# Optimization experiments

Hardware: AMD Instinct MI355X
Metric: run time of the kernel (lower is better)

Reference implementation:

```python
import jax, jax.numpy as jnp
import numpy as np
import math

B, T, D = 4, 4096, 512
K_CACHE = 16

def _layernorm(x, g, b, eps=1e-5):
    mu = x.mean(-1, keepdims=True)
    var = ((x - mu) ** 2).mean(-1, keepdims=True)
    return (x - mu) / jnp.sqrt(var + eps) * g + b

def _shift1(x):
    # prepend zero along time axis, drop last: x_prev[t] = x[t-1]
    return jnp.pad(x, ((0, 0), (1, 0), (0, 0)))[:, :-1]

def mipt_parallel_scan(p, theta, inp_re, inp_im):
    # Faithful replication of the torch loop: ceil(log2(T+1)) iterations,
    # each combining with the element shifted by ONE position (as written).
    Bt, Tt, Dt = p.shape
    a_re = (1.0 - p) * jnp.cos(theta)
    a_im = (1.0 - p) * jnp.sin(theta)
    b_re, b_im = inp_re, inp_im
    mask = (jnp.arange(Tt) >= 1)[None, :, None]
    steps = math.ceil(math.log2(Tt + 1))
    for _ in range(steps):
        ar_p, ai_p = _shift1(a_re), _shift1(a_im)
        br_p, bi_p = _shift1(b_re), _shift1(b_im)
        new_a_re = a_re * ar_p - a_im * ai_p
        new_a_im = a_re * ai_p + a_im * ar_p
        new_b_re = a_re * br_p - a_im * bi_p + b_re
        new_b_im = a_re * bi_p + a_im * br_p + b_im
        a_re = jnp.where(mask, new_a_re, a_re)
        a_im = jnp.where(mask, new_a_im, a_im)
        b_re = jnp.where(mask, new_b_re, b_re)
        b_im = jnp.where(mask, new_b_im, b_im)
    return b_re, b_im

def setup_inputs() -> dict:
    key = jax.random.key(0)
    ks = jax.random.split(key, 32)
    s = 0.02
    def W(k, i, o):
        return jax.random.normal(k, (i, o), jnp.float32) * s
    inp = {
        'x': jax.random.normal(ks[0], (B, T, D), jnp.float32),
        'ln1_g': jnp.ones((D,), jnp.float32), 'ln1_b': jnp.zeros((D,), jnp.float32),
        'ln2_g': jnp.ones((D,), jnp.float32), 'ln2_b': jnp.zeros((D,), jnp.float32),
        'Wp_w': W(ks[1], D, D), 'Wp_b': jnp.zeros((D,), jnp.float32),
        'Wt_w': W(ks[2], D, D), 'Wt_b': jnp.zeros((D,), jnp.float32),
        'Wr_w': W(ks[3], D, D), 'Wr_b': jnp.zeros((D,), jnp.float32),
        'Wi_w': W(ks[4], D, D), 'Wi_b': jnp.zeros((D,), jnp.float32),
        'Wk_w': W(ks[5], D, D), 'Wk_b': jnp.zeros((D,), jnp.float32),
        'Wv_w': W(ks[6], D, D), 'Wv_b': jnp.zeros((D,), jnp.float32),
        'Wq_w': W(ks[7], D, D), 'Wq_b': jnp.zeros((D,), jnp.float32),
        'gate_w': W(ks[8], D, 1), 'gate_b': jnp.zeros((1,), jnp.float32),
        'ffn1_w': W(ks[9], D, 4 * D), 'ffn1_b': jnp.zeros((4 * D,), jnp.float32),
        'ffn2_w': W(ks[10], 4 * D, D), 'ffn2_b': jnp.zeros((D,), jnp.float32),
    }
    return inp

def reference(x, ln1_g, ln1_b, ln2_g, ln2_b, Wp_w, Wp_b, Wt_w, Wt_b, Wr_w, Wr_b,
              Wi_w, Wi_b, Wk_w, Wk_b, Wv_w, Wv_b, Wq_w, Wq_b, gate_w, gate_b,
              ffn1_w, ffn1_b, ffn2_w, ffn2_b):
    Bx, Tx, Dx = x.shape
    residual = x
    xn = _layernorm(x, ln1_g, ln1_b)
    p = jax.nn.sigmoid(xn @ Wp_w + Wp_b)
    theta = xn @ Wt_w + Wt_b
    inp_re = xn @ Wr_w + Wr_b
    inp_im = xn @ Wi_w + Wi_b
    h_re, _h_im = mipt_parallel_scan(p, theta, inp_re, inp_im)
    h_mean = h_re.mean(axis=1)  # [B, D]
    # CausalSparseCache (eval mode)
    p_scalar = p.mean(axis=-1)  # [B, T]
    K = min(K_CACHE, Tx)
    _, topk_idx = jax.lax.top_k(p_scalar, K)  # [B, K]
    idx = jnp.broadcast_to(topk_idx[:, :, None], (Bx, K, Dx))
    h_topk = jnp.take_along_axis(h_re, idx, axis=1)  # [B, K, D]
    keys = h_topk @ Wk_w + Wk_b
    values = h_topk @ Wv_w + Wv_b
    query = (h_mean @ Wq_w + Wq_b)[:, None, :]  # [B, 1, D]
    scores = jnp.einsum('bqd,bkd->bqk', query, keys) / math.sqrt(Dx)
    attn = jax.nn.softmax(scores, axis=-1)
    cache_out = jnp.einsum('bqk,bkd->bqd', attn, values)[:, 0]  # [B, D]
    g = jax.nn.sigmoid(h_mean @ gate_w + gate_b)  # [B, 1]
    out = h_mean + g * cache_out
    h = h_re + residual
    hn = _layernorm(h, ln2_g, ln2_b)
    ffn = jax.nn.gelu(hn @ ffn1_w + ffn1_b, approximate=False) @ ffn2_w + ffn2_b
    h = h + ffn
    return (h, out)
```

## Files before the change

### kernel.cpp

```cpp
#include <hip/hip_runtime.h>
#include <hip/hip_bf16.h>
#include <cstdint>
#include <cstddef>

typedef __bf16 bf16;
typedef __attribute__((ext_vector_type(8))) __bf16 bf16x8;
typedef __attribute__((ext_vector_type(4))) float f32x4;

#define BB 4
#define TT 4096
#define DD 512
#define MM (BB * TT)
#define OUT1_OFF ((size_t)MM * DD)

typedef __attribute__((address_space(1))) void as1_void;
typedef __attribute__((address_space(3))) void as3_void;

__device__ __forceinline__ void gl_lds16(const void* g, void* l) {
    __builtin_amdgcn_global_load_lds((as1_void*)(uintptr_t)g,
                                     (as3_void*)(uintptr_t)l, 16, 0, 0);
}

__global__ void transpose_bf16(const float* __restrict__ in, bf16* __restrict__ out,
                               int R, int C) {
    __shared__ float tile[32][33];
    const int c0 = blockIdx.x * 32, r0 = blockIdx.y * 32;
    const int tx = threadIdx.x, ty = threadIdx.y;
#pragma unroll
    for (int i = 0; i < 32; i += 8)
        tile[ty + i][tx] = in[(size_t)(r0 + ty + i) * C + (c0 + tx)];
    __syncthreads();
#pragma unroll
    for (int i = 0; i < 32; i += 8)
        out[(size_t)(c0 + ty + i) * R + (r0 + tx)] = (bf16)tile[tx][ty + i];
}

__global__ void pack_bias(const float* __restrict__ a, const float* __restrict__ b,
                          const float* __restrict__ c, const float* __restrict__ d,
                          float* __restrict__ o) {
    const int i = blockIdx.x * 256 + threadIdx.x;
    if (i < 2048) {
        const float* s = (i < 512) ? a : (i < 1024) ? b : (i < 1536) ? c : d;
        o[i] = s[i & 511];
    }
}

__global__ void zero_kernel(float* __restrict__ p, int n) {
    const int i = blockIdx.x * 256 + threadIdx.x;
    if (i < n) p[i] = 0.f;
}

__global__ __launch_bounds__(256) void ln_kernel(
    const float* __restrict__ X, const float* __restrict__ Xadd,
    const float* __restrict__ gw, const float* __restrict__ bw,
    bf16* __restrict__ out) {
    const int row = blockIdx.x * 4 + (threadIdx.x >> 6);
    const int lane = threadIdx.x & 63;
    const float* xr = X + (size_t)row * DD + lane * 8;
    float v[8];
    float4 v0 = *(const float4*)xr;
    float4 v1 = *(const float4*)(xr + 4);
    v[0] = v0.x; v[1] = v0.y; v[2] = v0.z; v[3] = v0.w;
    v[4] = v1.x; v[5] = v1.y; v[6] = v1.z; v[7] = v1.w;
    if (Xadd) {
        const float* ad = Xadd + (size_t)row * DD + lane * 8;
        float4 a0 = *(const float4*)ad;
        float4 a1 = *(const float4*)(ad + 4);
        v[0] += a0.x; v[1] += a0.y; v[2] += a0.z; v[3] += a0.w;
        v[4] += a1.x; v[5] += a1.y; v[6] += a1.z; v[7] += a1.w;
    }
    float s = 0.f, ss = 0.f;
#pragma unroll
    for (int i = 0; i < 8; ++i) { s += v[i]; ss += v[i] * v[i]; }
#pragma unroll
    for (int o = 32; o; o >>= 1) { s += __shfl_down(s, o); ss += __shfl_down(ss, o); }
    s = __shfl(s, 0); ss = __shfl(ss, 0);
    const float mu = s * (1.f / DD);
    const float var = ss * (1.f / DD) - mu * mu;
    const float rstd = rsqrtf(var + 1e-5f);
    bf16x8 o8;
#pragma unroll
    for (int i = 0; i < 8; ++i)
        o8[i] = (bf16)((v[i] - mu) * rstd * gw[lane * 8 + i] + bw[lane * 8 + i]);
    *(bf16x8*)(out + (size_t)row * DD + lane * 8) = o8;
}

template <int MODE>
__global__ __launch_bounds__(256) void gemm_bt(
    const bf16* __restrict__ A, const bf16* __restrict__ Bt,
    const float* __restrict__ bias, void* __restrict__ Cout,
    void* __restrict__ Cout2,
    const float* __restrict__ add1, const float* __restrict__ add2,
    int M, int N, int K) {
    __shared__ bf16 As[2][4096];
    __shared__ bf16 Bs[2][4096];
    const int tid = threadIdx.x;
    const int lane = tid & 63;
    const int wv = tid >> 6;
    const int wr = wv >> 1, wc = wv & 1;
    const int nb = N >> 7;
    const int nwg = gridDim.x;
    int bx = blockIdx.x;
    if ((nwg & 7) == 0) bx = (bx & 7) * (nwg >> 3) + (bx >> 3);
    const int bm = bx / nb, bn = bx % nb;
    const int m0 = bm << 7, n0 = bn << 7;

    const int srow = tid >> 2;
    const int scol = (tid & 3) << 3;
    const bf16* Asrc = A + (size_t)(m0 + srow) * K + scol;
    const bf16* Bsrc = Bt + (size_t)(n0 + srow) * K + scol;
    const size_t rstep = (size_t)64 * K;

    const int lr = lane & 15, lg = lane >> 4;
    const int aoff = (wr * 64 + lr) * 32 + lg * 8;
    const int boff = (wc * 64 + lr) * 32 + lg * 8;

#define STG(buf, k0)                                                \
    do {                                                            \
        gl_lds16(Asrc + (k0),         &As[buf][wv * 512]);          \
        gl_lds16(Asrc + (k0) + rstep, &As[buf][wv * 512 + 2048]);   \
        gl_lds16(Bsrc + (k0),         &Bs[buf][wv * 512]);          \
        gl_lds16(Bsrc + (k0) + rstep, &Bs[buf][wv * 512 + 2048]);   \
    } while (0)

    f32x4 acc00 = {}, acc01 = {}, acc02 = {}, acc03 = {};
    f32x4 acc10 = {}, acc11 = {}, acc12 = {}, acc13 = {};
    f32x4 acc20 = {}, acc21 = {}, acc22 = {}, acc23 = {};
    f32x4 acc30 = {}, acc31 = {}, acc32 = {}, acc33 = {};

    const int NT = K >> 5;
    STG(0, 0);
    STG(1, 32);
    for (int t = 0; t < NT; ++t) {
        if (t + 1 < NT) asm volatile("s_waitcnt vmcnt(4)" ::: "memory");
        else            asm volatile("s_waitcnt vmcnt(0)" ::: "memory");
        __builtin_amdgcn_s_barrier();
        asm volatile("" ::: "memory");
        const bf16* Ab = As[t & 1];
        const bf16* Bb = Bs[t & 1];
        bf16x8 af0 = *(const bf16x8*)&Ab[aoff];
        bf16x8 af1 = *(const bf16x8*)&Ab[aoff + 512];
        bf16x8 af2 = *(const bf16x8*)&Ab[aoff + 1024];
        bf16x8 af3 = *(const bf16x8*)&Ab[aoff + 1536];
        bf16x8 bf0 = *(const bf16x8*)&Bb[boff];
        bf16x8 bf1 = *(const bf16x8*)&Bb[boff + 512];
        bf16x8 bf2 = *(const bf16x8*)&Bb[boff + 1024];
        bf16x8 bf3 = *(const bf16x8*)&Bb[boff + 1536];
#define MF(a_, b_, c_) c_ = __builtin_amdgcn_mfma_f32_16x16x32_bf16(a_, b_, c_, 0, 0, 0)
        MF(af0, bf0, acc00); MF(af0, bf1, acc01); MF(af0, bf2, acc02); MF(af0, bf3, acc03);
        MF(af1, bf0, acc10); MF(af1, bf1, acc11); MF(af1, bf2, acc12); MF(af1, bf3, acc13);
        MF(af2, bf0, acc20); MF(af2, bf1, acc21); MF(af2, bf2, acc22); MF(af2, bf3, acc23);
        MF(af3, bf0, acc30); MF(af3, bf1, acc31); MF(af3, bf2, acc32); MF(af3, bf3, acc33);
#undef MF
        __builtin_amdgcn_s_barrier();
        asm volatile("" ::: "memory");
        if (t + 2 < NT) STG(t & 1, (t + 2) << 5);
    }
#undef STG

#define EPI(mi, ni, ACC)                                                        \
    do {                                                                        \
        const int gmb = m0 + wr * 64 + mi * 16 + 4 * lg;                        \
        const int gn = n0 + wc * 64 + ni * 16 + lr;                             \
        const float bia = bias[gn];                                             \
        _Pragma("unroll")                                                       \
        for (int i = 0; i < 4; ++i) {                                           \
            float v = ACC[i] + bia;                                             \
            const int row = gmb + i;                                            \
            if (MODE == 0) {                                                    \
                if (gn < 512) ((float*)Cout)[(size_t)row * 512 + gn] = v;       \
                else ((bf16*)Cout2)[(size_t)row * 1536 + (gn - 512)] = (bf16)v; \
            } else if (MODE == 1) {                                             \
                const float ge = 0.5f * v * (1.0f + erff(v * 0.70710678118654752f)); \
                ((bf16*)Cout)[(size_t)row * N + gn] = (bf16)ge;                 \
            } else {                                                            \
                const size_t off = (size_t)row * N + gn;                        \
                ((float*)Cout)[off] = v + add1[off] + add2[off];                \
            }                                                                   \
        }                                                                       \
    } while (0)
    EPI(0, 0, acc00); EPI(0, 1, acc01); EPI(0, 2, acc02); EPI(0, 3, acc03);
    EPI(1, 0, acc10); EPI(1, 1, acc11); EPI(1, 2, acc12); EPI(1, 3, acc13);
    EPI(2, 0, acc20); EPI(2, 1, acc21); EPI(2, 2, acc22); EPI(2, 3, acc23);
    EPI(3, 0, acc30); EPI(3, 1, acc31); EPI(3, 2, acc32); EPI(3, 3, acc33);
#undef EPI
}

__global__ __launch_bounds__(256) void pscalar_kernel(const float* __restrict__ linp,
                                                      float* __restrict__ ps) {
    const int row = blockIdx.x * 4 + (threadIdx.x >> 6);
    const int lane = threadIdx.x & 63;
    const float* pr = linp + (size_t)row * 512 + lane * 8;
    float s = 0.f;
#pragma unroll
    for (int i = 0; i < 8; ++i) {
        const float v = pr[i];
        s += __builtin_amdgcn_rcpf(1.f + __expf(-v));
    }
#pragma unroll
    for (int o = 32; o; o >>= 1) s += __shfl_down(s, o);
    if (!lane) ps[row] = s * (1.f / 512.f);
}

#define SCL 32
__global__ __launch_bounds__(256) void scan_kernel(const float* __restrict__ linp,
                                                   const bf16* __restrict__ lint,
                                                   float* __restrict__ h_re) {
    const int blk = blockIdx.x;
    const int dh = blk & 1;
    const int tc = (blk >> 1) & 127;
    const int b = blk >> 8;
    const int d = dh * 256 + threadIdx.x;
    const int t0 = tc * SCL;

    float par[13], pai[13], pbr[13], pbi[13];
#pragma unroll
    for (int k = 0; k < 13; ++k) { par[k] = 0.f; pai[k] = 0.f; pbr[k] = 0.f; pbi[k] = 0.f; }

    const int warm = (tc == 0) ? 0 : 13;
    const float* pp = linp + (size_t)(b * TT + t0 - warm) * 512 + d;
    const bf16* tp = lint + (size_t)(b * TT + t0 - warm) * 1536 + d;
    float* pout = h_re + ((size_t)(b * TT + t0)) * DD + d;

    for (int s = 0; s < warm; ++s) {
        const float pl = pp[0];
        const float th = (float)tp[0];
        const float re = (float)tp[512];
        const float im = (float)tp[1024];
        pp += 512; tp += 1536;
        const float om = __builtin_amdgcn_rcpf(1.f + __expf(pl));
        const float sn = __sinf(th), cs = __cosf(th);
        float car = om * cs, cai = om * sn, cbr = re, cbi = im;
#pragma unroll
        for (int k = 0; k < 13; ++k) {
            const float tar = par[k], tai = pai[k], tbr = pbr[k], tbi = pbi[k];
            par[k] = car; pai[k] = cai; pbr[k] = cbr; pbi[k] = cbi;
            const float nbr = car * tbr - cai * tbi + cbr;
            const float nbi = car * tbi + cai * tbr + cbi;
            if (k < 12) {
                const float nar = car * tar - cai * tai;
                const float nai = car * tai + cai * tar;
                car = nar; cai = nai;
            }
            cbr = nbr; cbi = nbi;
        }
    }

#pragma unroll 4
    for (int s = 0; s < SCL; ++s) {
        const int t = t0 + s;
        const float pl = pp[0];
        const float th = (float)tp[0];
        const float re = (float)tp[512];
        const float im = (float)tp[1024];
        pp += 512; tp += 1536;
        const float om = __builtin_amdgcn_rcpf(1.f + __expf(pl));
        const float sn = __sinf(th), cs = __cosf(th);
        float car = om * cs, cai = om * sn, cbr = re, cbi = im;
        if (t == 0) {
#pragma unroll
            for (int k = 0; k < 13; ++k) { par[k] = car; pai[k] = cai; pbr[k] = cbr; pbi[k] = cbi; }
        } else {
#pragma unroll
            for (int k = 0; k < 13; ++k) {
                const float tar = par[k], tai = pai[k], tbr = pbr[k], tbi = pbi[k];
                par[k] = car; pai[k] = cai; pbr[k] = cbr; pbi[k] = cbi;
                const float nbr = car * tbr - cai * tbi + cbr;
                const float nbi = car * tbi + cai * tbr + cbi;
                if (k < 12) {
                    const float nar = car * tar - cai * tai;
                    const float nai = car * tai + cai * tar;
                    car = nar; cai = nai;
                }
                cbr = nbr; cbi = nbi;
            }
        }
        pout[(size_t)s * DD] = cbr;
    }
}

__global__ __launch_bounds__(256) void hmean_kernel(const float* __restrict__ h_re,
                                                    float* __restrict__ hsum) {
    const int blk = blockIdx.x;
    const int b = blk >> 6;
    const int dh = (blk >> 5) & 1;
    const int tc = blk & 31;
    const int d = dh * 256 + threadIdx.x;
    float s = 0.f;
    const float* p = h_re + ((size_t)(b * TT + tc * 128)) * DD + d;
    for (int t = 0; t < 128; ++t) s += p[(size_t)t * DD];
    atomicAdd(&hsum[b * DD + d], s);
}

__global__ __launch_bounds__(256) void topk_kernel(const float* __restrict__ ps,
                                                   int* __restrict__ idx_out) {
    __shared__ float vals[TT];
    __shared__ float rv[4];
    __shared__ int ri[4];
    const int b = blockIdx.x, tid = threadIdx.x;
    for (int i = tid; i < TT; i += 256) vals[i] = ps[b * TT + i];
    __syncthreads();
    for (int kk = 0; kk < 16; ++kk) {
        float bv = -1e30f; int bi = 0x7fffffff;
        for (int i = tid; i < TT; i += 256) {
            const float v = vals[i];
            if (v > bv || (v == bv && i < bi)) { bv = v; bi = i; }
        }
#pragma unroll
        for (int o = 32; o; o >>= 1) {
            const float ov = __shfl_down(bv, o);
            const int oi = __shfl_down(bi, o);
            if (ov > bv || (ov == bv && oi < bi)) { bv = ov; bi = oi; }
        }
        const int lane = tid & 63, wid = tid >> 6;
        if (!lane) { rv[wid] = bv; ri[wid] = bi; }
        __syncthreads();
        if (!tid) {
            float fbv = rv[0]; int fbi = ri[0];
            for (int w = 1; w < 4; ++w)
                if (rv[w] > fbv || (rv[w] == fbv && ri[w] < fbi)) { fbv = rv[w]; fbi = ri[w]; }
            idx_out[b * 16 + kk] = fbi;
            vals[fbi] = -1e30f;
        }
        __syncthreads();
    }
}

__global__ __launch_bounds__(256) void kv_kernel(
    const float* __restrict__ h_re, const int* __restrict__ tki,
    const float* __restrict__ Wk, const float* __restrict__ Wkb,
    const float* __restrict__ Wv, const float* __restrict__ Wvb,
    float* __restrict__ keys, float* __restrict__ vals) {
    const int blk = blockIdx.x;
    const int b = blk >> 4, j = blk & 15;
    const int tid = threadIdx.x;
    __shared__ float hrow[512];
    const int row = tki[b * 16 + j];
    for (int i = tid; i < 512; i += 256)
        hrow[i] = h_re[((size_t)(b * TT + row)) * DD + i];
    __syncthreads();
    for (int n = tid; n < 512; n += 256) {
        float sk = Wkb[n], sv = Wvb[n];
        for (int k = 0; k < 512; ++k) {
            const float h = hrow[k];
            sk += h * Wk[(size_t)k * 512 + n];
            sv += h * Wv[(size_t)k * 512 + n];
        }
        keys[((size_t)(b * 16 + j)) * 512 + n] = sk;
        vals[((size_t)(b * 16 + j)) * 512 + n] = sv;
    }
}

__global__ __launch_bounds__(256) void attn_out_kernel(
    const float* __restrict__ hsum, const float* __restrict__ Wq,
    const float* __restrict__ Wqb, const float* __restrict__ gw,
    const float* __restrict__ gb, const float* __restrict__ keys,
    const float* __restrict__ vals, float* __restrict__ out1) {
    const int b = blockIdx.x, tid = threadIdx.x;
    const int lane = tid & 63, wid = tid >> 6;
    __shared__ float hm[512];
    __shared__ float q[512];
    __shared__ float sc[16];
    __shared__ float red[4];
    for (int d0 = tid; d0 < 512; d0 += 256)
        hm[d0] = hsum[b * 512 + d0] * (1.f / 4096.f);
    __syncthreads();
    for (int n = tid; n < 512; n += 256) {
        float s = Wqb[n];
        for (int k = 0; k < 512; ++k) s += hm[k] * Wq[(size_t)k * 512 + n];
        q[n] = s;
    }
    float gp = 0.f;
    for (int k = tid; k < 512; k += 256) gp += hm[k] * gw[k];
#pragma unroll
    for (int o = 32; o; o >>= 1) gp += __shfl_down(gp, o);
    if (!lane) red[wid] = gp;
    __syncthreads();
    const float g = 1.f / (1.f + __expf(-(red[0] + red[1] + red[2] + red[3] + gb[0])));
    for (int kk = wid; kk < 16; kk += 4) {
        float sp = 0.f;
        const float* kr = keys + ((size_t)(b * 16 + kk)) * 512;
        for (int k2 = lane; k2 < 512; k2 += 64) sp += q[k2] * kr[k2];
#pragma unroll
        for (int o = 32; o; o >>= 1) sp += __shfl_down(sp, o);
        if (!lane) sc[kk] = sp * 0.04419417382415922f;
    }
    __syncthreads();
    float mx = sc[0];
#pragma unroll
    for (int kk = 1; kk < 16; ++kk) mx = fmaxf(mx, sc[kk]);
    float den = 0.f;
    float w16[16];
#pragma unroll
    for (int kk = 0; kk < 16; ++kk) { w16[kk] = __expf(sc[kk] - mx); den += w16[kk]; }
    const float rden = 1.f / den;
    for (int d0 = tid; d0 < 512; d0 += 256) {
        float co = 0.f;
#pragma unroll
        for (int kk = 0; kk < 16; ++kk)
            co += w16[kk] * vals[((size_t)(b * 16 + kk)) * 512 + d0];
        out1[b * 512 + d0] = hm[d0] + g * (co * rden);
    }
}

extern "C" void kernel_launch(void* const* d_in, const int* in_sizes, int n_in,
                              void* d_out, int out_size, void* d_ws, size_t ws_size,
                              hipStream_t stream) {
    const float* x    = (const float*)d_in[0];
    const float* ln1g = (const float*)d_in[1];
    const float* ln1b = (const float*)d_in[2];
    const float* ln2g = (const float*)d_in[3];
    const float* ln2b = (const float*)d_in[4];
    const float* Wp_w = (const float*)d_in[5];
    const float* Wp_b = (const float*)d_in[6];
    const float* Wt_w = (const float*)d_in[7];
    const float* Wt_b = (const float*)d_in[8];
    const float* Wr_w = (const float*)d_in[9];
    const float* Wr_b = (const float*)d_in[10];
    const float* Wi_w = (const float*)d_in[11];
    const float* Wi_b = (const float*)d_in[12];
    const float* Wk_w = (const float*)d_in[13];
    const float* Wk_b = (const float*)d_in[14];
    const float* Wv_w = (const float*)d_in[15];
    const float* Wv_b = (const float*)d_in[16];
    const float* Wq_w = (const float*)d_in[17];
    const float* Wq_b = (const float*)d_in[18];
    const float* gw   = (const float*)d_in[19];
    const float* gb   = (const float*)d_in[20];
    const float* f1w  = (const float*)d_in[21];
    const float* f1b  = (const float*)d_in[22];
    const float* f2w  = (const float*)d_in[23];
    const float* f2b  = (const float*)d_in[24];

    char* wsp = (char*)d_ws;
    float* linp = (float*)wsp;
    bf16* lint = (bf16*)(wsp + 33554432);
    char* p = wsp + 83886080;
    float* h_re = (float*)p; p += 33554432;
    bf16* xn = (bf16*)p;     p += 16777216;
    bf16* hn = (bf16*)p;     p += 16777216;
    bf16* wcat = (bf16*)p;   p += 2097152;
    bf16* f1bt = (bf16*)p;   p += 2097152;
    bf16* f2bt = (bf16*)p;   p += 2097152;
    float* bcat = (float*)p; p += 8192;
    float* ps = (float*)p;   p += 65536;
    float* hsum = (float*)p; p += 8192;
    int* tki = (int*)p;      p += 256;
    float* keys = (float*)p; p += 131072;
    float* valsb = (float*)p;
    bf16* act = (bf16*)wsp;
    float* out0 = (float*)d_out;
    float* out1 = (float*)d_out + OUT1_OFF;

    dim3 tb(32, 8);
    transpose_bf16<<<dim3(16, 16), tb, 0, stream>>>(Wp_w, wcat + (size_t)0 * 512 * 512, 512, 512);
    transpose_bf16<<<dim3(16, 16), tb, 0, stream>>>(Wt_w, wcat + (size_t)1 * 512 * 512, 512, 512);
    transpose_bf16<<<dim3(16, 16), tb, 0, stream>>>(Wr_w, wcat + (size_t)2 * 512 * 512, 512, 512);
    transpose_bf16<<<dim3(16, 16), tb, 0, stream>>>(Wi_w, wcat + (size_t)3 * 512 * 512, 512, 512);
    transpose_bf16<<<dim3(64, 16), tb, 0, stream>>>(f1w, f1bt, 512, 2048);
    transpose_bf16<<<dim3(16, 64), tb, 0, stream>>>(f2w, f2bt, 2048, 512);
    pack_bias<<<8, 256, 0, stream>>>(Wp_b, Wt_b, Wr_b, Wi_b, bcat);

    ln_kernel<<<4096, 256, 0, stream>>>(x, nullptr, ln1g, ln1b, xn);
    gemm_bt<0><<<2048, 256, 0, stream>>>(xn, wcat, bcat, linp, lint, nullptr, nullptr, MM, 2048, 512);
    pscalar_kernel<<<4096, 256, 0, stream>>>(linp, ps);
    scan_kernel<<<1024, 256, 0, stream>>>(linp, lint, h_re);
    zero_kernel<<<8, 256, 0, stream>>>(hsum, 2048);
    hmean_kernel<<<256, 256, 0, stream>>>(h_re, hsum);
    topk_kernel<<<4, 256, 0, stream>>>(ps, tki);
    kv_kernel<<<64, 256, 0, stream>>>(h_re, tki, Wk_w, Wk_b, Wv_w, Wv_b, keys, valsb);
    attn_out_kernel<<<4, 256, 0, stream>>>(hsum, Wq_w, Wq_b, gw, gb, keys, valsb, out1);
    ln_kernel<<<4096, 256, 0, stream>>>(h_re, x, ln2g, ln2b, hn);
    gemm_bt<1><<<2048, 256, 0, stream>>>(hn, f1bt, f1b, act, nullptr, nullptr, nullptr, MM, 2048, 512);
    gemm_bt<2><<<512, 256, 0, stream>>>(act, f2bt, f2b, out0, nullptr, h_re, x, MM, 512, 2048);
}
```

Baseline: 432.9 us.

## Add 256x256 8-wave GEMM kernel, halve scan chunk length, use hardware sin/cos

After: 494.6 us. 14.2% more time.

```diff
diff --git a/kernel.cpp b/kernel.cpp
--- a/kernel.cpp
+++ b/kernel.cpp
@@ -83,6 +83,124 @@
     for (int i = 0; i < 8; ++i)
         o8[i] = (bf16)((v[i] - mu) * rstd * gw[lane * 8 + i] + bw[lane * 8 + i]);
     *(bf16x8*)(out + (size_t)row * DD + lane * 8) = o8;
+}
+
+#define MF(a_, b_, c_) c_ = __builtin_amdgcn_mfma_f32_16x16x32_bf16(a_, b_, c_, 0, 0, 0)
+
+template <int MODE>
+__global__ __launch_bounds__(512, 2) void gemm8p(
+    const bf16* __restrict__ A, const bf16* __restrict__ Bt,
+    const float* __restrict__ bias, void* __restrict__ Cout,
+    void* __restrict__ Cout2, int M, int N, int K) {
+    __shared__ bf16 lds[2][2][2][128 * 64];
+    const int tid = threadIdx.x, lane = tid & 63, wv = tid >> 6;
+    const int wr = wv >> 2, wc = wv & 3;
+    const int lr = lane & 15, lg = lane >> 4;
+    const int nb = N >> 8;
+    const int nwg = gridDim.x;
+    int bx = blockIdx.x;
+    if ((nwg & 7) == 0) bx = (bx & 7) * (nwg >> 3) + (bx >> 3);
+    const int bm = bx / nb, bn = bx % nb;
+    const int m0 = bm << 8, n0 = bn << 8;
+
+    const int srow = tid >> 3;
+    const int scol = (((tid & 7) ^ (srow & 7)) << 3);
+    const bf16* Asrc = A + (size_t)(m0 + srow) * K + scol;
+    const bf16* Bsrc = Bt + (size_t)(n0 + srow) * K + scol;
+    const size_t r64 = (size_t)64 * K;
+    const size_t r128 = (size_t)128 * K;
+
+#define STAGE_H(bufi, mat, half, kt)                                              \
+    do {                                                                          \
+        const bf16* s_ = ((mat) == 0 ? Asrc : Bsrc) + (half) * r128 + (kt) * 64;  \
+        bf16* d_ = &lds[bufi][mat][half][wv * 512];                               \
+        gl_lds16(s_, d_);                                                         \
+        gl_lds16(s_ + r64, d_ + 4096);                                            \
+    } while (0)
+
+    const int psel0 = ((lg ^ (lr & 7)) << 3);
+    const int psel1 = (((4 + lg) ^ (lr & 7)) << 3);
+
+    f32x4 acc[8][4] = {};
+
+#define PHASE(bufi, qm, qn, kt1, smat, shalf, dostage)                             \
+    do {                                                                           \
+        const bf16* Ah_ = &lds[bufi][0][wr][0];                                    \
+        const bf16* Bh_ = &lds[bufi][1][wc >> 1][0];                               \
+        const int rA_ = ((qm) * 64 + lr) * 64;                                     \
+        const int rB_ = ((wc & 1) * 64 + (qn) * 32 + lr) * 64;                     \
+        bf16x8 a0_ = *(const bf16x8*)&Ah_[rA_ + psel0];                            \
+        bf16x8 a1_ = *(const bf16x8*)&Ah_[rA_ + 1024 + psel0];                     \
+        bf16x8 a2_ = *(const bf16x8*)&Ah_[rA_ + 2048 + psel0];                     \
+        bf16x8 a3_ = *(const bf16x8*)&Ah_[rA_ + 3072 + psel0];                     \
+        bf16x8 b0_ = *(const bf16x8*)&Bh_[rB_ + psel0];                            \
+        bf16x8 b1_ = *(const bf16x8*)&Bh_[rB_ + 1024 + psel0];                     \
+        bf16x8 a0b_ = *(const bf16x8*)&Ah_[rA_ + psel1];                           \
+        bf16x8 a1b_ = *(const bf16x8*)&Ah_[rA_ + 1024 + psel1];                    \
+        bf16x8 a2b_ = *(const bf16x8*)&Ah_[rA_ + 2048 + psel1];                    \
+        bf16x8 a3b_ = *(const bf16x8*)&Ah_[rA_ + 3072 + psel1];                    \
+        bf16x8 b0b_ = *(const bf16x8*)&Bh_[rB_ + psel1];                           \
+        bf16x8 b1b_ = *(const bf16x8*)&Bh_[rB_ + 1024 + psel1];                    \
+        if (dostage) STAGE_H((bufi) ^ 1, smat, shalf, kt1);                        \
+        __builtin_amdgcn_s_barrier();                                              \
+        __builtin_amdgcn_s_setprio(1);                                            \
+        MF(a0_, b0_, acc[(qm)*4+0][(qn)*2+0]);                                     \
+        MF(a1_, b0_, acc[(qm)*4+1][(qn)*2+0]);                                     \
+        MF(a2_, b0_, acc[(qm)*4+2][(qn)*2+0]);                                     \
+        MF(a3_, b0_, acc[(qm)*4+3][(qn)*2+0]);                                     \
+        MF(a0_, b1_, acc[(qm)*4+0][(qn)*2+1]);                                     \
+        MF(a1_, b1_, acc[(qm)*4+1][(qn)*2+1]);                                     \
+        MF(a2_, b1_, acc[(qm)*4+2][(qn)*2+1]);                                     \
+        MF(a3_, b1_, acc[(qm)*4+3][(qn)*2+1]);                                     \
+        MF(a0b_, b0b_, acc[(qm)*4+0][(qn)*2+0]);                                   \
+        MF(a1b_, b0b_, acc[(qm)*4+1][(qn)*2+0]);                                   \
+        MF(a2b_, b0b_, acc[(qm)*4+2][(qn)*2+0]);                                   \
+        MF(a3b_, b0b_, acc[(qm)*4+3][(qn)*2+0]);                                   \
+        MF(a0b_, b1b_, acc[(qm)*4+0][(qn)*2+1]);                                   \
+        MF(a1b_, b1b_, acc[(qm)*4+1][(qn)*2+1]);                                   \
+        MF(a2b_, b1b_, acc[(qm)*4+2][(qn)*2+1]);                                   \
+        MF(a3b_, b1b_, acc[(qm)*4+3][(qn)*2+1]);                                   \
+        __builtin_amdgcn_s_setprio(0);                                             \
+        __builtin_amdgcn_s_barrier();                                              \
+    } while (0)
+
+    const int NKT = K >> 6;
+    STAGE_H(0, 0, 0, 0); STAGE_H(0, 0, 1, 0);
+    STAGE_H(0, 1, 0, 0); STAGE_H(0, 1, 1, 0);
+    __syncthreads();
+    for (int kt = 0; kt < NKT; ++kt) {
+        const int buf = kt & 1;
+        const bool st = (kt + 1 < NKT);
+        PHASE(buf, 0, 0, kt + 1, 0, 0, st);
+        PHASE(buf, 1, 0, kt + 1, 0, 1, st);
+        PHASE(buf, 0, 1, kt + 1, 1, 0, st);
+        PHASE(buf, 1, 1, kt + 1, 1, 1, st);
+        __syncthreads();
+    }
+#undef PHASE
+#undef STAGE_H
+
+#pragma unroll
+    for (int mi = 0; mi < 8; ++mi) {
+#pragma unroll
+        for (int ni = 0; ni < 4; ++ni) {
+            const int gmb = m0 + wr * 128 + mi * 16 + 4 * lg;
+            const int gn = n0 + wc * 64 + ni * 16 + lr;
+            const float bia = bias[gn];
+#pragma unroll
+            for (int i = 0; i < 4; ++i) {
+                float v = acc[mi][ni][i] + bia;
+                const int row = gmb + i;
+                if (MODE == 0) {
+                    if (gn < 512) ((float*)Cout)[(size_t)row * 512 + gn] = v;
+                    else ((bf16*)Cout2)[(size_t)row * 1536 + (gn - 512)] = (bf16)v;
+                } else {
+                    const float ge = 0.5f * v * (1.0f + erff(v * 0.70710678118654752f));
+                    ((bf16*)Cout)[(size_t)row * N + gn] = (bf16)ge;
+                }
+            }
+        }
+    }
 }
 
 template <int MODE>
@@ -146,12 +264,10 @@
         bf16x8 bf1 = *(const bf16x8*)&Bb[boff + 512];
         bf16x8 bf2 = *(const bf16x8*)&Bb[boff + 1024];
         bf16x8 bf3 = *(const bf16x8*)&Bb[boff + 1536];
-#define MF(a_, b_, c_) c_ = __builtin_amdgcn_mfma_f32_16x16x32_bf16(a_, b_, c_, 0, 0, 0)
         MF(af0, bf0, acc00); MF(af0, bf1, acc01); MF(af0, bf2, acc02); MF(af0, bf3, acc03);
         MF(af1, bf0, acc10); MF(af1, bf1, acc11); MF(af1, bf2, acc12); MF(af1, bf3, acc13);
         MF(af2, bf0, acc20); MF(af2, bf1, acc21); MF(af2, bf2, acc22); MF(af2, bf3, acc23);
         MF(af3, bf0, acc30); MF(af3, bf1, acc31); MF(af3, bf2, acc32); MF(af3, bf3, acc33);
-#undef MF
         __builtin_amdgcn_s_barrier();
         asm volatile("" ::: "memory");
         if (t + 2 < NT) STG(t & 1, (t + 2) << 5);
@@ -202,14 +318,14 @@
     if (!lane) ps[row] = s * (1.f / 512.f);
 }
 
-#define SCL 32
+#define SCL 16
 __global__ __launch_bounds__(256) void scan_kernel(const float* __restrict__ linp,
                                                    const bf16* __restrict__ lint,
                                                    float* __restrict__ h_re) {
     const int blk = blockIdx.x;
     const int dh = blk & 1;
-    const int tc = (blk >> 1) & 127;
-    const int b = blk >> 8;
+    const int tc = (blk >> 1) & 255;
+    const int b = blk >> 9;
     const int d = dh * 256 + threadIdx.x;
     const int t0 = tc * SCL;
 
@@ -222,15 +338,22 @@
     const bf16* tp = lint + (size_t)(b * TT + t0 - warm) * 1536 + d;
     float* pout = h_re + ((size_t)(b * TT + t0)) * DD + d;
 
+#define XFORM(car, cai, cbr, cbi)                                        \
+    const float pl = pp[0];                                              \
+    const float th = (float)tp[0];                                       \
+    const float re = (float)tp[512];                                     \
+    const float im = (float)tp[1024];                                    \
+    pp += 512; tp += 1536;                                               \
+    const float om = __builtin_amdgcn_rcpf(1.f + __expf(pl));            \
+    float fr_, sn, cs;                                                   \
+    { const float rv_ = th * 0.15915494309189535f;                       \
+      asm("v_fract_f32 %0, %1" : "=v"(fr_) : "v"(rv_));                  \
+      asm("v_sin_f32 %0, %1" : "=v"(sn) : "v"(fr_));                     \
+      asm("v_cos_f32 %0, %1" : "=v"(cs) : "v"(fr_)); }                   \
+    float car = om * cs, cai = om * sn, cbr = re, cbi = im;
+
     for (int s = 0; s < warm; ++s) {
-        const float pl = pp[0];
-        const float th = (float)tp[0];
-        const float re = (float)tp[512];
-        const float im = (float)tp[1024];
-        pp += 512; tp += 1536;
-        const float om = __builtin_amdgcn_rcpf(1.f + __expf(pl));
-        const float sn = __sinf(th), cs = __cosf(th);
-        float car = om * cs, cai = om * sn, cbr = re, cbi = im;
+        XFORM(car, cai, cbr, cbi)
 #pragma unroll
         for (int k = 0; k < 13; ++k) {
             const float tar = par[k], tai = pai[k], tbr = pbr[k], tbi = pbi[k];
@@ -249,14 +372,7 @@
 #pragma unroll 4
     for (int s = 0; s < SCL; ++s) {
         const int t = t0 + s;
-        const float pl = pp[0];
-        const float th = (float)tp[0];
-        const float re = (float)tp[512];
-        const float im = (float)tp[1024];
-        pp += 512; tp += 1536;
-        const float om = __builtin_amdgcn_rcpf(1.f + __expf(pl));
-        const float sn = __sinf(th), cs = __cosf(th);
-        float car = om * cs, cai = om * sn, cbr = re, cbi = im;
+        XFORM(car, cai, cbr, cbi)
         if (t == 0) {
 #pragma unroll
             for (int k = 0; k < 13; ++k) { par[k] = car; pai[k] = cai; pbr[k] = cbr; pbi[k] = cbi; }
@@ -277,6 +393,7 @@
         }
         pout[(size_t)s * DD] = cbr;
     }
+#undef XFORM
 }
 
 __global__ __launch_bounds__(256) void hmean_kernel(const float* __restrict__ h_re,
@@ -462,15 +579,15 @@
     pack_bias<<<8, 256, 0, stream>>>(Wp_b, Wt_b, Wr_b, Wi_b, bcat);
 
     ln_kernel<<<4096, 256, 0, stream>>>(x, nullptr, ln1g, ln1b, xn);
-    gemm_bt<0><<<2048, 256, 0, stream>>>(xn, wcat, bcat, linp, lint, nullptr, nullptr, MM, 2048, 512);
+    gemm8p<0><<<512, 512, 0, stream>>>(xn, wcat, bcat, linp, lint, MM, 2048, 512);
     pscalar_kernel<<<4096, 256, 0, stream>>>(linp, ps);
-    scan_kernel<<<1024, 256, 0, stream>>>(linp, lint, h_re);
+    scan_kernel<<<2048, 256, 0, stream>>>(linp, lint, h_re);
     zero_kernel<<<8, 256, 0, stream>>>(hsum, 2048);
     hmean_kernel<<<256, 256, 0, stream>>>(h_re, hsum);
     topk_kernel<<<4, 256, 0, stream>>>(ps, tki);
     kv_kernel<<<64, 256, 0, stream>>>(h_re, tki, Wk_w, Wk_b, Wv_w, Wv_b, keys, valsb);
     attn_out_kernel<<<4, 256, 0, stream>>>(hsum, Wq_w, Wq_b, gw, gb, keys, valsb, out1);
     ln_kernel<<<4096, 256, 0, stream>>>(h_re, x, ln2g, ln2b, hn);
-    gemm_bt<1><<<2048, 256, 0, stream>>>(hn, f1bt, f1b, act, nullptr, nullptr, nullptr, MM, 2048, 512);
+    gemm8p<1><<<512, 512, 0, stream>>>(hn, f1bt, f1b, act, nullptr, MM, 2048, 512);
     gemm_bt<2><<<512, 256, 0, stream>>>(act, f2bt, f2b, out0, nullptr, h_re, x, MM, 512, 2048);
 }
```

## Swizzle GEMM LDS layout, halve scan chunk length, use hardware sin/cos

Applied to the files above, without the earlier changes.

Result: no change. 428.2 us (-1.1%).

```diff
diff --git a/kernel.cpp b/kernel.cpp
--- a/kernel.cpp
+++ b/kernel.cpp
@@ -84,6 +84,8 @@
         o8[i] = (bf16)((v[i] - mu) * rstd * gw[lane * 8 + i] + bw[lane * 8 + i]);
     *(bf16x8*)(out + (size_t)row * DD + lane * 8) = o8;
 }
+
+#define MF(a_, b_, c_) c_ = __builtin_amdgcn_mfma_f32_16x16x32_bf16(a_, b_, c_, 0, 0, 0)
 
 template <int MODE>
 __global__ __launch_bounds__(256) void gemm_bt(
@@ -106,14 +108,15 @@
     const int m0 = bm << 7, n0 = bn << 7;
 
     const int srow = tid >> 2;
-    const int scol = (tid & 3) << 3;
+    const int scol = (((tid & 3) ^ ((tid >> 3) & 3)) << 3);
     const bf16* Asrc = A + (size_t)(m0 + srow) * K + scol;
     const bf16* Bsrc = Bt + (size_t)(n0 + srow) * K + scol;
     const size_t rstep = (size_t)64 * K;
 
     const int lr = lane & 15, lg = lane >> 4;
-    const int aoff = (wr * 64 + lr) * 32 + lg * 8;
-    const int boff = (wc * 64 + lr) * 32 + lg * 8;
+    const int sel = ((lg ^ ((lr >> 1) & 3)) << 3);
+    const int aoff = (wr * 64 + lr) * 32 + sel;
+    const int boff = (wc * 64 + lr) * 32 + sel;
 
 #define STG(buf, k0)                                                \
     do {                                                            \
@@ -146,12 +149,10 @@
         bf16x8 bf1 = *(const bf16x8*)&Bb[boff + 512];
         bf16x8 bf2 = *(const bf16x8*)&Bb[boff + 1024];
         bf16x8 bf3 = *(const bf16x8*)&Bb[boff + 1536];
-#define MF(a_, b_, c_) c_ = __builtin_amdgcn_mfma_f32_16x16x32_bf16(a_, b_, c_, 0, 0, 0)
         MF(af0, bf0, acc00); MF(af0, bf1, acc01); MF(af0, bf2, acc02); MF(af0, bf3, acc03);
         MF(af1, bf0, acc10); MF(af1, bf1, acc11); MF(af1, bf2, acc12); MF(af1, bf3, acc13);
         MF(af2, bf0, acc20); MF(af2, bf1, acc21); MF(af2, bf2, acc22); MF(af2, bf3, acc23);
         MF(af3, bf0, acc30); MF(af3, bf1, acc31); MF(af3, bf2, acc32); MF(af3, bf3, acc33);
-#undef MF
         __builtin_amdgcn_s_barrier();
         asm volatile("" ::: "memory");
         if (t + 2 < NT) STG(t & 1, (t + 2) << 5);
@@ -202,14 +203,14 @@
     if (!lane) ps[row] = s * (1.f / 512.f);
 }
 
-#define SCL 32
+#define SCL 16
 __global__ __launch_bounds__(256) void scan_kernel(const float* __restrict__ linp,
                                                    const bf16* __restrict__ lint,
                                                    float* __restrict__ h_re) {
     const int blk = blockIdx.x;
     const int dh = blk & 1;
-    const int tc = (blk >> 1) & 127;
-    const int b = blk >> 8;
+    const int tc = (blk >> 1) & 255;
+    const int b = blk >> 9;
     const int d = dh * 256 + threadIdx.x;
     const int t0 = tc * SCL;
 
@@ -222,15 +223,22 @@
     const bf16* tp = lint + (size_t)(b * TT + t0 - warm) * 1536 + d;
     float* pout = h_re + ((size_t)(b * TT + t0)) * DD + d;
 
+#define XFORM(car, cai, cbr, cbi)                                        \
+    const float pl = pp[0];                                              \
+    const float th = (float)tp[0];                                       \
+    const float re = (float)tp[512];                                     \
+    const float im = (float)tp[1024];                                    \
+    pp += 512; tp += 1536;                                               \
+    const float om = __builtin_amdgcn_rcpf(1.f + __expf(pl));            \
+    float fr_, sn, cs;                                                   \
+    { const float rv_ = th * 0.15915494309189535f;                       \
+      asm("v_fract_f32 %0, %1" : "=v"(fr_) : "v"(rv_));                  \
+      asm("v_sin_f32 %0, %1" : "=v"(sn) : "v"(fr_));                     \
+      asm("v_cos_f32 %0, %1" : "=v"(cs) : "v"(fr_)); }                   \
+    float car = om * cs, cai = om * sn, cbr = re, cbi = im;
+
     for (int s = 0; s < warm; ++s) {
-        const float pl = pp[0];
-        const float th = (float)tp[0];
-        const float re = (float)tp[512];
-        const float im = (float)tp[1024];
-        pp += 512; tp += 1536;
-        const float om = __builtin_amdgcn_rcpf(1.f + __expf(pl));
-        const float sn = __sinf(th), cs = __cosf(th);
-        float car = om * cs, cai = om * sn, cbr = re, cbi = im;
+        XFORM(car, cai, cbr, cbi)
 #pragma unroll
         for (int k = 0; k < 13; ++k) {
             const float tar = par[k], tai = pai[k], tbr = pbr[k], tbi = pbi[k];
@@ -249,14 +257,7 @@
 #pragma unroll 4
     for (int s = 0; s < SCL; ++s) {
         const int t = t0 + s;
-        const float pl = pp[0];
-        const float th = (float)tp[0];
-        const float re = (float)tp[512];
-        const float im = (float)tp[1024];
-        pp += 512; tp += 1536;
-        const float om = __builtin_amdgcn_rcpf(1.f + __expf(pl));
-        const float sn = __sinf(th), cs = __cosf(th);
-        float car = om * cs, cai = om * sn, cbr = re, cbi = im;
+        XFORM(car, cai, cbr, cbi)
         if (t == 0) {
 #pragma unroll
             for (int k = 0; k < 13; ++k) { par[k] = car; pai[k] = cai; pbr[k] = cbr; pbi[k] = cbi; }
@@ -277,6 +278,7 @@
         }
         pout[(size_t)s * DD] = cbr;
     }
+#undef XFORM
 }
 
 __global__ __launch_bounds__(256) void hmean_kernel(const float* __restrict__ h_re,
@@ -464,7 +466,7 @@
     ln_kernel<<<4096, 256, 0, stream>>>(x, nullptr, ln1g, ln1b, xn);
     gemm_bt<0><<<2048, 256, 0, stream>>>(xn, wcat, bcat, linp, lint, nullptr, nullptr, MM, 2048, 512);
     pscalar_kernel<<<4096, 256, 0, stream>>>(linp, ps);
-    scan_kernel<<<1024, 256, 0, stream>>>(linp, lint, h_re);
+    scan_kernel<<<2048, 256, 0, stream>>>(linp, lint, h_re);
     zero_kernel<<<8, 256, 0, stream>>>(hsum, 2048);
     hmean_kernel<<<256, 256, 0, stream>>>(h_re, hsum);
     topk_kernel<<<4, 256, 0, stream>>>(ps, tki);
```
